# Optimization experiments

Hardware: AMD Instinct MI355X
Metric: run time of the kernel (lower is better)

## Reference

```python
import jax, jax.numpy as jnp
import numpy as np

B, T, IN, H = 512, 2048, 2, 128


def setup_inputs() -> dict:
    key = jax.random.key(0)
    ks = jax.random.split(key, 14)
    u = lambda k, shape: jax.random.uniform(k, shape, jnp.float32, -0.1, 0.1)
    return {
        "x": jax.random.normal(ks[0], (B, T, IN), jnp.float32),
        "mask": jnp.ones((B, T), jnp.float32),
        "emb_W": u(ks[1], (H, IN)), "emb_b": u(ks[2], (H,)),
        "enc_W": u(ks[3], (H, H)), "enc_b": u(ks[4], (H,)),
        "dec_input": u(ks[5], (H,)), "Vec": u(ks[6], (H,)),
        "Wq_W": u(ks[7], (H, H)), "Wq_b": u(ks[8], (H,)),
        "Wref_W": u(ks[9], (H, H)), "Wref_b": u(ks[10], (H,)),
        "fc1_W": u(ks[11], (H, H)), "fc2_W": u(ks[12], (2, H)),
    }


def reference(x, mask, emb_W, emb_b, enc_W, enc_b, dec_input, Vec,
              Wq_W, Wq_b, Wref_W, Wref_b, fc1_W, fc2_W):
    # Embedding: (B,T,IN) -> (B,T,H)
    x_embed = jnp.einsum("bti,hi->bth", x, emb_W) + emb_b
    # Encoder (stand-in for external Encoder class): per-token Linear + mask
    ref = (jnp.einsum("bti,hi->bth", x_embed, enc_W) + enc_b) * mask[:, :, None]

    def glimpse(query, ref):
        # query: (B,H); ref: (B,T,H)
        u1 = query @ Wq_W.T + Wq_b                                  # (B,H)
        # Conv1d kernel size 1 == pointwise linear over hidden dim
        u2 = jnp.einsum("bti,oi->bot", ref, Wref_W) + Wref_b[None, :, None]  # (B,H,T)
        u = jnp.einsum("h,bht->bt", Vec, jnp.tanh(u1[:, :, None] + u2))      # (B,T)
        a = jax.nn.softmax(u, axis=1)                               # (B,T)
        return jnp.einsum("bht,bt->bh", u2, a)                      # (B,H)

    query = jnp.broadcast_to(dec_input, (x.shape[0], dec_input.shape[0]))
    for _ in range(2):
        query = glimpse(query, ref)

    # final2FC: Linear(no bias) -> ReLU -> Linear(no bias); squeeze(-1) twice is a no-op (last dim=2)
    pred_l = jax.nn.relu(query @ fc1_W.T) @ fc2_W.T                 # (B,2)
    return pred_l
```

## Files before the change

kernel.cpp:

```cpp
#include <hip/hip_runtime.h>
#include <hip/hip_bf16.h>


#define Bsz 512
#define Tsz 2048
#define Hsz 128
#define THR 256
#define TOK 4
#define QB 2
static_assert(QB * THR * TOK == Tsz, "token tiling must cover each row exactly");

#define C2LOG2E 2.8853900817779268f
#define LOG2E   1.4426950408889634f

__device__ __forceinline__ float exp2fast(float x) { return __builtin_amdgcn_exp2f(x); }
__device__ __forceinline__ float rcpfast(float x)  { return __builtin_amdgcn_rcpf(x); }

__global__ __launch_bounds__(128) void kprep(
        const float* __restrict__ embW, const float* __restrict__ embB,
        const float* __restrict__ encW, const float* __restrict__ encB,
        const float* __restrict__ wrefW, const float* __restrict__ wrefB,
        const float* __restrict__ wqW, const float* __restrict__ wqB,
        const float* __restrict__ dec, const float* __restrict__ vec,
        float4* __restrict__ SCA, float4* __restrict__ UC, float* __restrict__ V2G) {
    __shared__ float m0[Hsz], m1[Hsz], cc[Hsz], dq[Hsz];
    int h = threadIdx.x;
    float a0 = 0.f, a1 = 0.f, ac = 0.f;
    for (int k = 0; k < Hsz; ++k) {
        float w = encW[h * Hsz + k];
        a0 = fmaf(w, embW[2 * k + 0], a0);
        a1 = fmaf(w, embW[2 * k + 1], a1);
        ac = fmaf(w, embB[k], ac);
    }
    m0[h] = a0; m1[h] = a1; cc[h] = ac + encB[h]; dq[h] = dec[h];
    __syncthreads();
    float p0 = 0.f, p1 = 0.f, pe = 0.f, uq = wqB[h];
    for (int k = 0; k < Hsz; ++k) {
        float w = wrefW[h * Hsz + k];
        p0 = fmaf(w, m0[k], p0);
        p1 = fmaf(w, m1[k], p1);
        pe = fmaf(w, cc[k], pe);
        uq = fmaf(wqW[h * Hsz + k], dq[k], uq);
    }
    float wb = wrefB[h];
    SCA[h] = make_float4(C2LOG2E * p0, C2LOG2E * p1, C2LOG2E * pe, C2LOG2E * (uq + wb));
    UC[h]  = make_float4(p0, p1, pe, wb);
    V2G[h] = 2.f * vec[h];
}

__global__ __launch_bounds__(THR) void kscore(
        const float* __restrict__ x, const float* __restrict__ mask,
        const float4* __restrict__ quadG, int bstride,
        const float* __restrict__ V2G,
        float4* __restrict__ statsOut) {
    __shared__ float4 quad[Hsz];
    __shared__ float v2s[Hsz];
    __shared__ float4 wr4[THR / 64];
    int blk = blockIdx.x, tid = threadIdx.x;
    int b = blk >> 1, qb = blk & 1;
    int wave = tid >> 6, lane = tid & 63;
    if (tid < Hsz) {
        quad[tid] = quadG[(size_t)b * bstride + tid];
        v2s[tid] = V2G[tid];
    }

    size_t tok0 = (size_t)b * Tsz + (size_t)qb * (THR * TOK);
    const float2* x2 = (const float2*)(x + tok0 * 2);
    const float* mrow = mask + tok0;
    float xm0[TOK], xm1[TOK], mk[TOK];
    #pragma unroll
    for (int j = 0; j < TOK; ++j) {
        float2 xv = x2[j * THR + tid];
        float m = mrow[j * THR + tid];
        mk[j] = m; xm0[j] = xv.x * m; xm1[j] = xv.y * m;
    }
    __syncthreads();

    float acc[TOK] = {0.f, 0.f, 0.f, 0.f};
    #pragma unroll 4
    for (int h = 0; h < Hsz; ++h) {
        float4 qd = quad[h];
        float vv = v2s[h];
        #pragma unroll
        for (int j = 0; j < TOK; ++j) {
            float a = fmaf(xm0[j], qd.x, fmaf(xm1[j], qd.y, fmaf(mk[j], qd.z, qd.w)));
            acc[j] = fmaf(vv, rcpfast(exp2fast(a) + 1.f), acc[j]);
        }
    }

    float Z = 0.f, Sm = 0.f, S0 = 0.f, S1 = 0.f;
    #pragma unroll
    for (int j = 0; j < TOK; ++j) {
        float e = exp2fast(-LOG2E * acc[j]);
        Z += e;
        Sm = fmaf(e, mk[j], Sm);
        S0 = fmaf(e, xm0[j], S0);
        S1 = fmaf(e, xm1[j], S1);
    }
    for (int off = 32; off; off >>= 1) {
        Z += __shfl_xor(Z, off); Sm += __shfl_xor(Sm, off);
        S0 += __shfl_xor(S0, off); S1 += __shfl_xor(S1, off);
    }
    if (lane == 0) wr4[wave] = make_float4(Z, Sm, S0, S1);
    __syncthreads();
    if (tid == 0) {
        float4 s = wr4[0];
        #pragma unroll
        for (int w = 1; w < THR / 64; ++w) {
            s.x += wr4[w].x; s.y += wr4[w].y; s.z += wr4[w].z; s.w += wr4[w].w;
        }
        statsOut[blk] = s;
    }
}

__global__ __launch_bounds__(128) void kmid(
        const float4* __restrict__ statsA, const float4* __restrict__ UC,
        const float4* __restrict__ SCA,
        const float* __restrict__ wqW, const float* __restrict__ wqB,
        float4* __restrict__ QB1) {
    __shared__ float q[Hsz];
    int b = blockIdx.x, tid = threadIdx.x;
    float Z = 0.f, Sm = 0.f, S0 = 0.f, S1 = 0.f;
    #pragma unroll
    for (int i = 0; i < QB; ++i) {
        float4 t = statsA[b * QB + i];
        Z += t.x; Sm += t.y; S0 += t.z; S1 += t.w;
    }
    float inv = 1.f / Z;
    float X0 = S0 * inv, X1 = S1 * inv, Cm = Sm * inv;
    float4 u4 = UC[tid];
    q[tid] = fmaf(X0, u4.x, fmaf(X1, u4.y, fmaf(Cm, u4.z, u4.w)));
    __syncthreads();
    float s = wqB[tid];
    const float* wr = wqW + (size_t)tid * Hsz;
    #pragma unroll 8
    for (int k = 0; k < Hsz; ++k) s = fmaf(wr[k], q[k], s);
    float4 sc = SCA[tid];
    QB1[b * Hsz + tid] = make_float4(sc.x, sc.y, sc.z, C2LOG2E * (s + u4.w));
}

__global__ __launch_bounds__(128) void kfin(
        const float4* __restrict__ statsB, const float4* __restrict__ UC,
        const float* __restrict__ fc1, const float* __restrict__ fc2,
        float* __restrict__ out) {
    __shared__ float q[Hsz], rr[Hsz];
    int b = blockIdx.x, tid = threadIdx.x;
    float Z = 0.f, Sm = 0.f, S0 = 0.f, S1 = 0.f;
    #pragma unroll
    for (int i = 0; i < QB; ++i) {
        float4 t = statsB[b * QB + i];
        Z += t.x; Sm += t.y; S0 += t.z; S1 += t.w;
    }
    float inv = 1.f / Z;
    float X0 = S0 * inv, X1 = S1 * inv, Cm = Sm * inv;
    float4 u4 = UC[tid];
    q[tid] = fmaf(X0, u4.x, fmaf(X1, u4.y, fmaf(Cm, u4.z, u4.w)));
    __syncthreads();
    float s = 0.f;
    const float* fr = fc1 + (size_t)tid * Hsz;
    #pragma unroll 8
    for (int k = 0; k < Hsz; ++k) s = fmaf(fr[k], q[k], s);
    rr[tid] = fmaxf(s, 0.f);
    __syncthreads();
    int o = tid >> 6, l = tid & 63;
    float s2 = fc2[o * Hsz + l] * rr[l] + fc2[o * Hsz + 64 + l] * rr[64 + l];
    for (int off = 32; off; off >>= 1) s2 += __shfl_xor(s2, off);
    if (l == 0) out[b * 2 + o] = s2;
}

extern "C" void kernel_launch(void* const* d_in, const int* in_sizes, int n_in,
                              void* d_out, int out_size, void* d_ws, size_t ws_size,
                              hipStream_t stream) {
    const float* x     = (const float*)d_in[0];
    const float* mask  = (const float*)d_in[1];
    const float* embW  = (const float*)d_in[2];
    const float* embB  = (const float*)d_in[3];
    const float* encW  = (const float*)d_in[4];
    const float* encB  = (const float*)d_in[5];
    const float* dec   = (const float*)d_in[6];
    const float* vec   = (const float*)d_in[7];
    const float* wqW   = (const float*)d_in[8];
    const float* wqB   = (const float*)d_in[9];
    const float* wrefW = (const float*)d_in[10];
    const float* wrefB = (const float*)d_in[11];
    const float* fc1   = (const float*)d_in[12];
    const float* fc2   = (const float*)d_in[13];

    float* ws = (float*)d_ws;
    float4* SCA    = (float4*)(ws + 0);
    float4* UC     = (float4*)(ws + 512);
    float*  V2G    = ws + 1024;
    float4* QB1    = (float4*)(ws + 1536);
    float4* statsA = (float4*)(ws + 263680);
    float4* statsB = (float4*)(ws + 267776);
    float* out = (float*)d_out;

    kprep<<<1, 128, 0, stream>>>(embW, embB, encW, encB, wrefW, wrefB, wqW, wqB,
                                 dec, vec, SCA, UC, V2G);
    kscore<<<Bsz * QB, THR, 0, stream>>>(x, mask, SCA, 0, V2G, statsA);
    kmid<<<Bsz, 128, 0, stream>>>(statsA, UC, SCA, wqW, wqB, QB1);
    kscore<<<Bsz * QB, THR, 0, stream>>>(x, mask, QB1, Hsz, V2G, statsB);
    kfin<<<Bsz, 128, 0, stream>>>(statsB, UC, fc1, fc2, out);
}
```

Before: 92.19 us.

## Fuse mid query projection into second score pass and batch reciprocals by four

Removes the separate kmid kernel: each block of the second score pass now rebuilds its batch row's query from the first-pass stats and runs the Wq matvec itself, so the QB1 buffer and one launch disappear. The inner tanh-sum loop is also restructured to combine four sigmoid terms over a common denominator, using one reciprocal per four hidden units instead of four. The cost is that the Wq matvec is computed twice per batch row, once in each of its two blocks. The combined product of four (exp+1) terms risks overflow for large pre-activations.

New measurement: 90.71 us. About the same (-1.6%).

```diff
diff --git a/kernel.cpp b/kernel.cpp
--- a/kernel.cpp
+++ b/kernel.cpp
@@ -48,21 +48,23 @@
     V2G[h] = 2.f * vec[h];
 }
 
+template<bool MID>
 __global__ __launch_bounds__(THR) void kscore(
         const float* __restrict__ x, const float* __restrict__ mask,
-        const float4* __restrict__ quadG, int bstride,
-        const float* __restrict__ V2G,
+        const float4* __restrict__ SCA, const float* __restrict__ V2G,
+        const float4* __restrict__ UC,
+        const float* __restrict__ wqW, const float* __restrict__ wqB,
+        const float4* __restrict__ statsIn,
         float4* __restrict__ statsOut) {
     __shared__ float4 quad[Hsz];
-    __shared__ float v2s[Hsz];
+    __shared__ float4 v4s[Hsz / 4];
+    __shared__ float qv[Hsz];
     __shared__ float4 wr4[THR / 64];
     int blk = blockIdx.x, tid = threadIdx.x;
     int b = blk >> 1, qb = blk & 1;
     int wave = tid >> 6, lane = tid & 63;
-    if (tid < Hsz) {
-        quad[tid] = quadG[(size_t)b * bstride + tid];
-        v2s[tid] = V2G[tid];
-    }
+    if (tid < Hsz) quad[tid] = SCA[tid];
+    if (tid < Hsz / 4) v4s[tid] = ((const float4*)V2G)[tid];
 
     size_t tok0 = (size_t)b * Tsz + (size_t)qb * (THR * TOK);
     const float2* x2 = (const float2*)(x + tok0 * 2);
@@ -74,17 +76,52 @@
         float m = mrow[j * THR + tid];
         mk[j] = m; xm0[j] = xv.x * m; xm1[j] = xv.y * m;
     }
+
+    if (MID) {
+        float Zc = 0.f, Smc = 0.f, S0c = 0.f, S1c = 0.f;
+        #pragma unroll
+        for (int i = 0; i < QB; ++i) {
+            float4 t = statsIn[b * QB + i];
+            Zc += t.x; Smc += t.y; S0c += t.z; S1c += t.w;
+        }
+        float inv = 1.f / Zc;
+        float X0 = S0c * inv, X1 = S1c * inv, Cm = Smc * inv;
+        if (tid < Hsz) {
+            float4 u4 = UC[tid];
+            qv[tid] = fmaf(X0, u4.x, fmaf(X1, u4.y, fmaf(Cm, u4.z, u4.w)));
+        }
+        __syncthreads();
+        if (tid < Hsz) {
+            float s = wqB[tid];
+            const float* wr = wqW + (size_t)tid * Hsz;
+            #pragma unroll 8
+            for (int k = 0; k < Hsz; ++k) s = fmaf(wr[k], qv[k], s);
+            quad[tid].w = C2LOG2E * (s + UC[tid].w);
+        }
+    }
     __syncthreads();
 
     float acc[TOK] = {0.f, 0.f, 0.f, 0.f};
-    #pragma unroll 4
-    for (int h = 0; h < Hsz; ++h) {
-        float4 qd = quad[h];
-        float vv = v2s[h];
+    #pragma unroll 2
+    for (int g = 0; g < Hsz / 4; ++g) {
+        float4 q0 = quad[4 * g], q1 = quad[4 * g + 1];
+        float4 q2 = quad[4 * g + 2], q3 = quad[4 * g + 3];
+        float4 vv = v4s[g];
         #pragma unroll
         for (int j = 0; j < TOK; ++j) {
-            float a = fmaf(xm0[j], qd.x, fmaf(xm1[j], qd.y, fmaf(mk[j], qd.z, qd.w)));
-            acc[j] = fmaf(vv, rcpfast(exp2fast(a) + 1.f), acc[j]);
+            float p0 = fmaf(xm0[j], q0.x, fmaf(xm1[j], q0.y, fmaf(mk[j], q0.z, q0.w)));
+            float p1 = fmaf(xm0[j], q1.x, fmaf(xm1[j], q1.y, fmaf(mk[j], q1.z, q1.w)));
+            float p2 = fmaf(xm0[j], q2.x, fmaf(xm1[j], q2.y, fmaf(mk[j], q2.z, q2.w)));
+            float p3 = fmaf(xm0[j], q3.x, fmaf(xm1[j], q3.y, fmaf(mk[j], q3.z, q3.w)));
+            float f0 = exp2fast(p0) + 1.f;
+            float f1 = exp2fast(p1) + 1.f;
+            float f2 = exp2fast(p2) + 1.f;
+            float f3 = exp2fast(p3) + 1.f;
+            float AB = f0 * f1, CD = f2 * f3;
+            float h01 = fmaf(vv.x, f1, vv.y * f0);
+            float h23 = fmaf(vv.z, f3, vv.w * f2);
+            float num = fmaf(h01, CD, h23 * AB);
+            acc[j] = fmaf(num, rcpfast(AB * CD), acc[j]);
         }
     }
 
@@ -111,32 +148,6 @@
         }
         statsOut[blk] = s;
     }
-}
-
-__global__ __launch_bounds__(128) void kmid(
-        const float4* __restrict__ statsA, const float4* __restrict__ UC,
-        const float4* __restrict__ SCA,
-        const float* __restrict__ wqW, const float* __restrict__ wqB,
-        float4* __restrict__ QB1) {
-    __shared__ float q[Hsz];
-    int b = blockIdx.x, tid = threadIdx.x;
-    float Z = 0.f, Sm = 0.f, S0 = 0.f, S1 = 0.f;
-    #pragma unroll
-    for (int i = 0; i < QB; ++i) {
-        float4 t = statsA[b * QB + i];
-        Z += t.x; Sm += t.y; S0 += t.z; S1 += t.w;
-    }
-    float inv = 1.f / Z;
-    float X0 = S0 * inv, X1 = S1 * inv, Cm = Sm * inv;
-    float4 u4 = UC[tid];
-    q[tid] = fmaf(X0, u4.x, fmaf(X1, u4.y, fmaf(Cm, u4.z, u4.w)));
-    __syncthreads();
-    float s = wqB[tid];
-    const float* wr = wqW + (size_t)tid * Hsz;
-    #pragma unroll 8
-    for (int k = 0; k < Hsz; ++k) s = fmaf(wr[k], q[k], s);
-    float4 sc = SCA[tid];
-    QB1[b * Hsz + tid] = make_float4(sc.x, sc.y, sc.z, C2LOG2E * (s + u4.w));
 }
 
 __global__ __launch_bounds__(128) void kfin(
@@ -190,15 +201,15 @@
     float4* SCA    = (float4*)(ws + 0);
     float4* UC     = (float4*)(ws + 512);
     float*  V2G    = ws + 1024;
-    float4* QB1    = (float4*)(ws + 1536);
-    float4* statsA = (float4*)(ws + 263680);
-    float4* statsB = (float4*)(ws + 267776);
+    float4* statsA = (float4*)(ws + 1536);
+    float4* statsB = (float4*)(ws + 5632);
     float* out = (float*)d_out;
 
     kprep<<<1, 128, 0, stream>>>(embW, embB, encW, encB, wrefW, wrefB, wqW, wqB,
                                  dec, vec, SCA, UC, V2G);
-    kscore<<<Bsz * QB, THR, 0, stream>>>(x, mask, SCA, 0, V2G, statsA);
-    kmid<<<Bsz, 128, 0, stream>>>(statsA, UC, SCA, wqW, wqB, QB1);
-    kscore<<<Bsz * QB, THR, 0, stream>>>(x, mask, QB1, Hsz, V2G, statsB);
+    kscore<false><<<Bsz * QB, THR, 0, stream>>>(x, mask, SCA, V2G, UC, wqW, wqB,
+                                                nullptr, statsA);
+    kscore<true><<<Bsz * QB, THR, 0, stream>>>(x, mask, SCA, V2G, UC, wqW, wqB,
+                                               statsA, statsB);
     kfin<<<Bsz, 128, 0, stream>>>(statsB, UC, fc1, fc2, out);
 }
```
